# Optimization experiments

Measured on AMD Instinct MI355X. Metric: run time of the kernel, lower is better.

The kernel has to match this reference:

```python
import jax, jax.numpy as jnp
import numpy as np

_SCAN_CHUNK = 32


def _causal_decay_scan(x, decay, init):
    """Inclusive scan out[t] = decay*out[t-1] + x[t], chunked closed form.
    x: [B,H,T,D], decay: [1,H,1], init: [B,H,D]. Returns [B,H,T,D]."""
    B, H, T, D = x.shape
    C = min(_SCAN_CHUNK, T)
    assert T % C == 0
    nC = T // C
    log_decay = jnp.log(jnp.clip(decay.astype(jnp.float32), 1e-8, None))  # [1,H,1]
    c_idx = jnp.arange(C, dtype=jnp.float32)
    log_p = log_decay[..., None] * c_idx.reshape(1, 1, C, 1)              # [1,H,C,1]
    p = jnp.exp(log_p)
    inv_p = jnp.exp(-log_p)
    init_p = jnp.exp(log_decay[..., None] * (c_idx + 1.0).reshape(1, 1, C, 1))
    # [nC, B, H, C, D] so lax.scan chains chunk states causally
    xc = x.reshape(B, H, nC, C, D).transpose(2, 0, 1, 3, 4).astype(jnp.float32)

    def step(state, chunk):  # state [B,H,D], chunk [B,H,C,D]
        cs = jnp.cumsum(chunk * inv_p, axis=2)
        out = cs * p + state[:, :, None, :] * init_p
        return out[:, :, -1, :], out

    _, outs = jax.lax.scan(step, init.astype(jnp.float32), xc)
    return outs.transpose(1, 2, 0, 3, 4).reshape(B, H, T, D).astype(x.dtype)


def _phi(x):
    return jax.nn.elu(x) + 1.0


def setup_inputs() -> dict:
    key = jax.random.key(0)
    ks = jax.random.split(key, 5)
    B, T, hidden, H = 4, 4096, 1024, 16
    s = 1.0 / np.sqrt(hidden)
    x = jax.random.normal(ks[0], (B, T, hidden), dtype=jnp.float32)
    Wqkv = jax.random.normal(ks[1], (3 * hidden, hidden), dtype=jnp.float32) * s
    Wout = jax.random.normal(ks[2], (hidden, hidden), dtype=jnp.float32) * s
    Wgate = jax.random.normal(ks[3], (hidden, hidden), dtype=jnp.float32) * s
    bgate = jnp.zeros((hidden,), dtype=jnp.float32)
    logit = float(np.log(0.95 / 0.05))  # sigmoid(logit) == 0.95
    decay_param = jnp.full((H,), logit, dtype=jnp.float32)
    return {"x": x, "Wqkv": Wqkv, "Wout": Wout, "Wgate": Wgate,
            "bgate": bgate, "decay_param": decay_param}


def reference(x, Wqkv, Wout, Wgate, bgate, decay_param):
    B, T, hidden = x.shape
    H = decay_param.shape[0]
    D = hidden // H
    qkv = x @ Wqkv.T                       # [B,T,3*hidden]
    q, k, v = jnp.split(qkv, 3, axis=-1)
    # [B,T,hidden] -> [B,H,T,D]
    q = q.reshape(B, T, H, D).transpose(0, 2, 1, 3)
    k = k.reshape(B, T, H, D).transpose(0, 2, 1, 3)
    v = v.reshape(B, T, H, D).transpose(0, 2, 1, 3)
    q = _phi(q)
    k = _phi(k)
    decay = jax.nn.sigmoid(decay_param).reshape(1, H, 1)
    kv_init = jnp.zeros((B, H, D), dtype=x.dtype)
    ksum_init = jnp.zeros((B, H, D), dtype=x.dtype)
    running_kv = _causal_decay_scan(k * v, decay, kv_init)
    running_ksum = _causal_decay_scan(k, decay, ksum_init)
    den = jnp.clip(jnp.sum(q * running_ksum, axis=-1, keepdims=True), 1e-6, None)
    out = q * running_kv / den             # [B,H,T,D]
    v_direct = v.transpose(0, 2, 1, 3).reshape(B, T, hidden)
    out = out.transpose(0, 2, 1, 3).reshape(B, T, hidden)
    g = jax.nn.sigmoid(out @ Wgate.T + bgate)
    out = g * out + (1.0 - g) * v_direct
    return out @ Wout.T
```

## Files before the change

kernel.cpp:

```cpp
#include <hip/hip_runtime.h>

typedef unsigned short u16;
typedef __bf16 bf16x8 __attribute__((ext_vector_type(8)));
typedef float f32x4 __attribute__((ext_vector_type(4)));
typedef unsigned short us8 __attribute__((ext_vector_type(8)));

#define BB 4
#define TT 4096
#define HID 1024
#define NH 16
#define HD 64
#define BT (BB*TT)
#define NCH 128
#define LOG_NCH 7
#define CLEN (TT/NCH)

__device__ __forceinline__ float bf2f(u16 u) {
    return __uint_as_float(((unsigned)u) << 16);
}
__device__ __forceinline__ u16 f2bf(float f) {
    unsigned u = __float_as_uint(f);
    unsigned r = 0x7FFFu + ((u >> 16) & 1u);
    return (u16)((u + r) >> 16);
}
__device__ __forceinline__ float phi(float x) {
    return x > 0.f ? x + 1.f : __expf(x);
}
__device__ __forceinline__ float sigmoidf(float x) {
    return 1.f / (1.f + __expf(-x));
}
__device__ __forceinline__ float4 u4_to_f4(ushort4 u) {
    return make_float4(bf2f(u.x), bf2f(u.y), bf2f(u.z), bf2f(u.w));
}

#define CN1 (BT*HID/4)
#define CN2 (3*HID*HID/4)
#define CN3 (HID*HID/4)
#define CN4 (HID*HID/4)
__global__ void convert_all(const float4* __restrict__ x,    const float4* __restrict__ wqkv,
                            const float4* __restrict__ wgate, const float4* __restrict__ wout,
                            ushort4* __restrict__ xb,    ushort4* __restrict__ wqkvb,
                            ushort4* __restrict__ wgateb, ushort4* __restrict__ woutb) {
    int i = blockIdx.x * 256 + threadIdx.x;
    const float4* src; ushort4* dst; int j;
    if (i < CN1)                 { src = x;     dst = xb;     j = i; }
    else if (i < CN1+CN2)        { src = wqkv;  dst = wqkvb;  j = i - CN1; }
    else if (i < CN1+CN2+CN3)    { src = wgate; dst = wgateb; j = i - CN1 - CN2; }
    else                         { src = wout;  dst = woutb;  j = i - CN1 - CN2 - CN3; }
    float4 f = src[j];
    ushort4 u;
    u.x = f2bf(f.x); u.y = f2bf(f.y); u.z = f2bf(f.z); u.w = f2bf(f.w);
    dst[j] = u;
}

__global__ __launch_bounds__(256)
void gemm_bt(const u16* __restrict__ A, const u16* __restrict__ Bm,
             int M, int N, int K, u16* __restrict__ Cout)
{
    __shared__ u16 As[128 * 64];
    __shared__ u16 Bs[128 * 64];
    const int tid  = threadIdx.x;
    const int wave = tid >> 6;
    const int lane = tid & 63;

    const int lin   = blockIdx.y * gridDim.x + blockIdx.x;
    const int xcd   = lin & 7;
    const int seq   = lin >> 3;
    const int bands = gridDim.y >> 3;
    const int my_by = xcd * bands + (seq % bands);
    const int my_bx = seq / bands;
    const int m0 = my_by * 128;
    const int n0 = my_bx * 128;

    const int mw = (wave & 1) * 64;
    const int nw = (wave >> 1) * 64;
    const int r16 = lane & 15;
    const int q4  = (lane >> 4) * 4;

    f32x4 acc[4][4];
    #pragma unroll
    for (int i = 0; i < 4; ++i)
        #pragma unroll
        for (int j = 0; j < 4; ++j)
            acc[i][j] = (f32x4){0.f, 0.f, 0.f, 0.f};

    for (int k0 = 0; k0 < K; k0 += 64) {
        #pragma unroll
        for (int i = 0; i < 4; ++i) {
            int s   = i * 4 + wave;
            int idx = s * 64 + lane;
            int pr  = idx >> 3;
            int pc  = idx & 7;
            int lc  = pc ^ (pr & 7);
            const u16* gA = A  + (size_t)(m0 + pr) * K + k0 + lc * 8;
            const u16* gB = Bm + (size_t)(n0 + pr) * K + k0 + lc * 8;
            __builtin_amdgcn_global_load_lds(
                (const __attribute__((address_space(1))) void*)gA,
                (__attribute__((address_space(3))) void*)&As[s * 512], 16, 0, 0);
            __builtin_amdgcn_global_load_lds(
                (const __attribute__((address_space(1))) void*)gB,
                (__attribute__((address_space(3))) void*)&Bs[s * 512], 16, 0, 0);
        }
        __syncthreads();
        #pragma unroll
        for (int s2 = 0; s2 < 2; ++s2) {
            const int lcq = s2 * 4 + (lane >> 4);
            const int pcq = lcq ^ (r16 & 7);
            bf16x8 af[4], bq[4];
            #pragma unroll
            for (int i = 0; i < 4; ++i)
                af[i] = *(const bf16x8*)&As[(mw + i * 16 + r16) * 64 + pcq * 8];
            #pragma unroll
            for (int j = 0; j < 4; ++j)
                bq[j] = *(const bf16x8*)&Bs[(nw + j * 16 + r16) * 64 + pcq * 8];
            #pragma unroll
            for (int i = 0; i < 4; ++i)
                #pragma unroll
                for (int j = 0; j < 4; ++j)
                    acc[i][j] = __builtin_amdgcn_mfma_f32_16x16x32_bf16(af[i], bq[j], acc[i][j], 0, 0, 0);
        }
        __syncthreads();
    }

    float* Cs = (float*)As;
    #pragma unroll
    for (int slab = 0; slab < 4; ++slab) {
        if ((mw == 64) == (slab >= 2)) {
            int i0 = (slab & 1) * 2;
            #pragma unroll
            for (int ii = 0; ii < 2; ++ii) {
                #pragma unroll
                for (int j = 0; j < 4; ++j) {
                    int col = nw + j * 16 + r16;
                    #pragma unroll
                    for (int r = 0; r < 4; ++r)
                        Cs[(ii * 16 + q4 + r) * 128 + col] = acc[i0 + ii][j][r];
                }
            }
        }
        __syncthreads();
        #pragma unroll
        for (int s = 0; s < 2; ++s) {
            int g   = s * 256 + tid;
            int row = g >> 4;
            int cg  = g & 15;
            const float* cp = &Cs[row * 128 + cg * 8];
            us8 o;
            #pragma unroll
            for (int e = 0; e < 8; ++e) o[e] = f2bf(cp[e]);
            size_t grow = (size_t)(m0 + slab * 32 + row);
            *(us8*)&Cout[grow * N + n0 + cg * 8] = o;
        }
        __syncthreads();
    }
}

template<int EPI>
__global__ __launch_bounds__(256)
void gemm_bt_sm(const u16* __restrict__ A, const u16* __restrict__ Bm,
                int M, int N, int K, void* __restrict__ Cout,
                const float* __restrict__ bg,
                const u16* __restrict__ attn,
                const u16* __restrict__ qkv)
{
    __shared__ u16 As[64 * 64];
    __shared__ u16 Bs[128 * 64];
    const int tid  = threadIdx.x;
    const int wave = tid >> 6;
    const int lane = tid & 63;

    const int lin   = blockIdx.y * gridDim.x + blockIdx.x;
    const int xcd   = lin & 7;
    const int seq   = lin >> 3;
    const int bands = gridDim.y >> 3;
    const int my_by = xcd * bands + (seq % bands);
    const int my_bx = seq / bands;
    const int m0 = my_by * 64;
    const int n0 = my_bx * 128;

    const int mw = (wave & 1) * 32;
    const int nw = (wave >> 1) * 64;
    const int r16 = lane & 15;
    const int q4  = (lane >> 4) * 4;

    f32x4 acc[2][4];
    #pragma unroll
    for (int i = 0; i < 2; ++i)
        #pragma unroll
        for (int j = 0; j < 4; ++j)
            acc[i][j] = (f32x4){0.f, 0.f, 0.f, 0.f};

    for (int k0 = 0; k0 < K; k0 += 64) {
        #pragma unroll
        for (int i = 0; i < 4; ++i) {
            int s   = i * 4 + wave;
            int idx = s * 64 + lane;
            int pr  = idx >> 3;
            int pc  = idx & 7;
            int lc  = pc ^ (pr & 7);
            const u16* gB = Bm + (size_t)(n0 + pr) * K + k0 + lc * 8;
            __builtin_amdgcn_global_load_lds(
                (const __attribute__((address_space(1))) void*)gB,
                (__attribute__((address_space(3))) void*)&Bs[s * 512], 16, 0, 0);
            if (i < 2) {
                const u16* gA = A + (size_t)(m0 + pr) * K + k0 + lc * 8;
                __builtin_amdgcn_global_load_lds(
                    (const __attribute__((address_space(1))) void*)gA,
                    (__attribute__((address_space(3))) void*)&As[s * 512], 16, 0, 0);
            }
        }
        __syncthreads();
        #pragma unroll
        for (int s2 = 0; s2 < 2; ++s2) {
            const int lcq = s2 * 4 + (lane >> 4);
            const int pcq = lcq ^ (r16 & 7);
            bf16x8 af[2], bq[4];
            #pragma unroll
            for (int i = 0; i < 2; ++i)
                af[i] = *(const bf16x8*)&As[(mw + i * 16 + r16) * 64 + pcq * 8];
            #pragma unroll
            for (int j = 0; j < 4; ++j)
                bq[j] = *(const bf16x8*)&Bs[(nw + j * 16 + r16) * 64 + pcq * 8];
            #pragma unroll
            for (int i = 0; i < 2; ++i)
                #pragma unroll
                for (int j = 0; j < 4; ++j)
                    acc[i][j] = __builtin_amdgcn_mfma_f32_16x16x32_bf16(af[i], bq[j], acc[i][j], 0, 0, 0);
        }
        __syncthreads();
    }

    float* Cs = (float*)Bs;
    #pragma unroll
    for (int slab = 0; slab < 2; ++slab) {
        if ((wave & 1) == slab) {
            #pragma unroll
            for (int i = 0; i < 2; ++i) {
                #pragma unroll
                for (int j = 0; j < 4; ++j) {
                    int col = nw + j * 16 + r16;
                    #pragma unroll
                    for (int r = 0; r < 4; ++r)
                        Cs[(i * 16 + q4 + r) * 128 + col] = acc[i][j][r];
                }
            }
        }
        __syncthreads();
        #pragma unroll
        for (int s = 0; s < 2; ++s) {
            int g   = s * 256 + tid;
            int row = g >> 4;
            int cg  = g & 15;
            const float* cp = &Cs[row * 128 + cg * 8];
            size_t grow = (size_t)(m0 + slab * 32 + row);
            int gcol = n0 + cg * 8;
            if (EPI == 1) {
                us8 a8 = *(const us8*)&attn[grow * HID + gcol];
                us8 v8 = *(const us8*)&qkv[grow * (3 * HID) + 2 * HID + gcol];
                us8 o;
                #pragma unroll
                for (int e = 0; e < 8; ++e) {
                    float gv = sigmoidf(cp[e] + bg[gcol + e]);
                    o[e] = f2bf(gv * bf2f(a8[e]) + (1.f - gv) * bf2f(v8[e]));
                }
                *(us8*)&((u16*)Cout)[grow * HID + gcol] = o;
            } else {
                float4 c0 = *(const float4*)cp;
                float4 c1 = *(const float4*)(cp + 4);
                float* op = &((float*)Cout)[grow * N + gcol];
                *(float4*)op = c0;
                *(float4*)(op + 4) = c1;
            }
        }
        __syncthreads();
    }
}

__global__ void scan_finals(const u16* __restrict__ qkv, const float* __restrict__ decay_param,
                            float* __restrict__ ckv, float* __restrict__ cks) {
    int g  = blockIdx.x * 16 + (threadIdx.x >> 4);
    int sl = threadIdx.x & 15;
    int c = g & (NCH - 1);
    int h = (g >> LOG_NCH) & (NH - 1);
    int b = g >> (LOG_NCH + 4);
    float decay = sigmoidf(decay_param[h]);
    const u16* kp = qkv + (size_t)(b * TT + c * CLEN) * (3 * HID) + HID + h * HD + sl * 4;
    float4 skv = make_float4(0.f, 0.f, 0.f, 0.f);
    float4 sks = make_float4(0.f, 0.f, 0.f, 0.f);
    for (int t = 0; t < CLEN; ++t) {
        float4 k = u4_to_f4(*(const ushort4*)kp);
        float4 v = u4_to_f4(*(const ushort4*)(kp + HID));
        k.x = phi(k.x); k.y = phi(k.y); k.z = phi(k.z); k.w = phi(k.w);
        skv.x = decay * skv.x + k.x * v.x;  skv.y = decay * skv.y + k.y * v.y;
        skv.z = decay * skv.z + k.z * v.z;  skv.w = decay * skv.w + k.w * v.w;
        sks.x = decay * sks.x + k.x;        sks.y = decay * sks.y + k.y;
        sks.z = decay * sks.z + k.z;        sks.w = decay * sks.w + k.w;
        kp += 3 * HID;
    }
    *(float4*)(ckv + (size_t)g * 64 + sl * 4) = skv;
    *(float4*)(cks + (size_t)g * 64 + sl * 4) = sks;
}

__global__ void scan_prefix(float* __restrict__ ckv, float* __restrict__ cks,
                            const float* __restrict__ decay_param) {
    int bh = blockIdx.x;
    int h  = bh & (NH - 1);
    int lane = threadIdx.x;
    float decay = sigmoidf(decay_param[h]);
    float dC = powf(decay, (float)CLEN);
    float* pkv = ckv + (size_t)bh * NCH * 64 + lane;
    float* pks = cks + (size_t)bh * NCH * 64 + lane;
    float fkv = 0.f, fks = 0.f;
    for (int c = 0; c < NCH; ++c) {
        float lkv = pkv[c * 64], lks = pks[c * 64];
        pkv[c * 64] = fkv; pks[c * 64] = fks;
        fkv = fkv * dC + lkv;
        fks = fks * dC + lks;
    }
}

__global__ void scan_apply(const u16* __restrict__ qkv, const float* __restrict__ decay_param,
                           const float* __restrict__ ckv, const float* __restrict__ cks,
                           u16* __restrict__ attn) {
    int g  = blockIdx.x * 16 + (threadIdx.x >> 4);
    int sl = threadIdx.x & 15;
    int c = g & (NCH - 1);
    int h = (g >> LOG_NCH) & (NH - 1);
    int b = g >> (LOG_NCH + 4);
    float decay = sigmoidf(decay_param[h]);
    float4 skv = *(const float4*)(ckv + (size_t)g * 64 + sl * 4);
    float4 sks = *(const float4*)(cks + (size_t)g * 64 + sl * 4);
    const u16* qp = qkv + (size_t)(b * TT + c * CLEN) * (3 * HID) + h * HD + sl * 4;
    u16* op = attn + (size_t)(b * TT + c * CLEN) * HID + h * HD + sl * 4;
    for (int t = 0; t < CLEN; ++t) {
        float4 q = u4_to_f4(*(const ushort4*)qp);
        float4 k = u4_to_f4(*(const ushort4*)(qp + HID));
        float4 v = u4_to_f4(*(const ushort4*)(qp + 2 * HID));
        q.x = phi(q.x); q.y = phi(q.y); q.z = phi(q.z); q.w = phi(q.w);
        k.x = phi(k.x); k.y = phi(k.y); k.z = phi(k.z); k.w = phi(k.w);
        skv.x = decay * skv.x + k.x * v.x;  skv.y = decay * skv.y + k.y * v.y;
        skv.z = decay * skv.z + k.z * v.z;  skv.w = decay * skv.w + k.w * v.w;
        sks.x = decay * sks.x + k.x;        sks.y = decay * sks.y + k.y;
        sks.z = decay * sks.z + k.z;        sks.w = decay * sks.w + k.w;
        float s = q.x * sks.x + q.y * sks.y + q.z * sks.z + q.w * sks.w;
        s += __shfl_xor(s, 8);
        s += __shfl_xor(s, 4);
        s += __shfl_xor(s, 2);
        s += __shfl_xor(s, 1);
        float inv = 1.f / fmaxf(s, 1e-6f);
        ushort4 o;
        o.x = f2bf(q.x * skv.x * inv); o.y = f2bf(q.y * skv.y * inv);
        o.z = f2bf(q.z * skv.z * inv); o.w = f2bf(q.w * skv.w * inv);
        *(ushort4*)op = o;
        qp += 3 * HID;
        op += HID;
    }
}

extern "C" void kernel_launch(void* const* d_in, const int* in_sizes, int n_in,
                              void* d_out, int out_size, void* d_ws, size_t ws_size,
                              hipStream_t stream) {
    const float* x     = (const float*)d_in[0];
    const float* Wqkv  = (const float*)d_in[1];
    const float* Wout  = (const float*)d_in[2];
    const float* Wgate = (const float*)d_in[3];
    const float* bgate = (const float*)d_in[4];
    const float* decay = (const float*)d_in[5];

    u16* xb     = (u16*)d_ws;
    u16* wqkvb  = xb    + (size_t)BT * HID;
    u16* wgateb = wqkvb + (size_t)3 * HID * HID;
    u16* woutb  = wgateb + (size_t)HID * HID;
    u16* qkvb   = woutb + (size_t)HID * HID;
    u16* out2b  = qkvb  + (size_t)BT * 3 * HID;
    float* ckv  = (float*)(out2b + (size_t)BT * HID);
    float* cks  = ckv + (size_t)BB * NH * NCH * HD;
    u16* attnb  = xb;

    convert_all<<<(CN1 + CN2 + CN3 + CN4) / 256, 256, 0, stream>>>(
        (const float4*)x, (const float4*)Wqkv, (const float4*)Wgate, (const float4*)Wout,
        (ushort4*)xb, (ushort4*)wqkvb, (ushort4*)wgateb, (ushort4*)woutb);

    gemm_bt<<<dim3(3 * HID / 128, BT / 128), 256, 0, stream>>>(
        xb, wqkvb, BT, 3 * HID, HID, qkvb);

    scan_finals<<<BB * NH * NCH / 16, 256, 0, stream>>>(qkvb, decay, ckv, cks);
    scan_prefix<<<BB * NH, 64, 0, stream>>>(ckv, cks, decay);
    scan_apply<<<BB * NH * NCH / 16, 256, 0, stream>>>(qkvb, decay, ckv, cks, attnb);

    gemm_bt_sm<1><<<dim3(HID / 128, BT / 64), 256, 0, stream>>>(
        attnb, wgateb, BT, HID, HID, out2b, bgate, attnb, qkvb);

    gemm_bt_sm<2><<<dim3(HID / 128, BT / 64), 256, 0, stream>>>(
        out2b, woutb, BT, HID, HID, d_out, nullptr, nullptr, nullptr);
}
```

Measured before the change: 423.5 us.

## Drop XCD block remap, write GEMM output directly, widen K tile to 128

Both GEMM kernels drop the XCD-aware block-index remapping and use plain blockIdx tile coordinates. The QKV GEMM replaces its LDS-staged, vectorized bf16 epilogue with direct per-element stores from the accumulators, which removes shared-memory round trips and barriers but leaves the global writes narrow. The small-M GEMM doubles its K tile to 128, halving loop iterations and barriers at the cost of more LDS. It also pads the C staging stride to cut bank conflicts and loads the gate bias as float4 vectors. Losing the remap may reduce L2 locality across XCDs.

```diff
diff --git a/kernel.cpp b/kernel.cpp
--- a/kernel.cpp
+++ b/kernel.cpp
@@ -62,20 +62,11 @@
     const int tid  = threadIdx.x;
     const int wave = tid >> 6;
     const int lane = tid & 63;
-
-    const int lin   = blockIdx.y * gridDim.x + blockIdx.x;
-    const int xcd   = lin & 7;
-    const int seq   = lin >> 3;
-    const int bands = gridDim.y >> 3;
-    const int my_by = xcd * bands + (seq % bands);
-    const int my_bx = seq / bands;
-    const int m0 = my_by * 128;
-    const int n0 = my_bx * 128;
-
+    const int m0 = blockIdx.y * 128;
+    const int n0 = blockIdx.x * 128;
     const int mw = (wave & 1) * 64;
     const int nw = (wave >> 1) * 64;
     const int r16 = lane & 15;
-    const int q4  = (lane >> 4) * 4;
 
     f32x4 acc[4][4];
     #pragma unroll
@@ -122,39 +113,20 @@
         __syncthreads();
     }
 
-    float* Cs = (float*)As;
     #pragma unroll
-    for (int slab = 0; slab < 4; ++slab) {
-        if ((mw == 64) == (slab >= 2)) {
-            int i0 = (slab & 1) * 2;
-            #pragma unroll
-            for (int ii = 0; ii < 2; ++ii) {
-                #pragma unroll
-                for (int j = 0; j < 4; ++j) {
-                    int col = nw + j * 16 + r16;
-                    #pragma unroll
-                    for (int r = 0; r < 4; ++r)
-                        Cs[(ii * 16 + q4 + r) * 128 + col] = acc[i0 + ii][j][r];
-                }
-            }
-        }
-        __syncthreads();
-        #pragma unroll
-        for (int s = 0; s < 2; ++s) {
-            int g   = s * 256 + tid;
-            int row = g >> 4;
-            int cg  = g & 15;
-            const float* cp = &Cs[row * 128 + cg * 8];
-            us8 o;
-            #pragma unroll
-            for (int e = 0; e < 8; ++e) o[e] = f2bf(cp[e]);
-            size_t grow = (size_t)(m0 + slab * 32 + row);
-            *(us8*)&Cout[grow * N + n0 + cg * 8] = o;
-        }
-        __syncthreads();
-    }
-}
-
+    for (int i = 0; i < 4; ++i) {
+        int rowb = m0 + mw + i * 16 + (lane >> 4) * 4;
+        #pragma unroll
+        for (int j = 0; j < 4; ++j) {
+            int col = n0 + nw + j * 16 + r16;
+            #pragma unroll
+            for (int r = 0; r < 4; ++r)
+                Cout[(size_t)(rowb + r) * N + col] = f2bf(acc[i][j][r]);
+        }
+    }
+}
+
+#define CS_LD 132
 template<int EPI>
 __global__ __launch_bounds__(256)
 void gemm_bt_sm(const u16* __restrict__ A, const u16* __restrict__ Bm,
@@ -163,21 +135,13 @@
                 const u16* __restrict__ attn,
                 const u16* __restrict__ qkv)
 {
-    __shared__ u16 As[64 * 64];
-    __shared__ u16 Bs[128 * 64];
+    __shared__ u16 As[64 * 128];
+    __shared__ u16 Bs[128 * 128];
     const int tid  = threadIdx.x;
     const int wave = tid >> 6;
     const int lane = tid & 63;
-
-    const int lin   = blockIdx.y * gridDim.x + blockIdx.x;
-    const int xcd   = lin & 7;
-    const int seq   = lin >> 3;
-    const int bands = gridDim.y >> 3;
-    const int my_by = xcd * bands + (seq % bands);
-    const int my_bx = seq / bands;
-    const int m0 = my_by * 64;
-    const int n0 = my_bx * 128;
-
+    const int m0 = blockIdx.y * 64;
+    const int n0 = blockIdx.x * 128;
     const int mw = (wave & 1) * 32;
     const int nw = (wave >> 1) * 64;
     const int r16 = lane & 15;
@@ -190,19 +154,19 @@
         for (int j = 0; j < 4; ++j)
             acc[i][j] = (f32x4){0.f, 0.f, 0.f, 0.f};
 
-    for (int k0 = 0; k0 < K; k0 += 64) {
-        #pragma unroll
-        for (int i = 0; i < 4; ++i) {
+    for (int k0 = 0; k0 < K; k0 += 128) {
+        #pragma unroll
+        for (int i = 0; i < 8; ++i) {
             int s   = i * 4 + wave;
             int idx = s * 64 + lane;
-            int pr  = idx >> 3;
-            int pc  = idx & 7;
+            int pr  = idx >> 4;
+            int pc  = idx & 15;
             int lc  = pc ^ (pr & 7);
             const u16* gB = Bm + (size_t)(n0 + pr) * K + k0 + lc * 8;
             __builtin_amdgcn_global_load_lds(
                 (const __attribute__((address_space(1))) void*)gB,
                 (__attribute__((address_space(3))) void*)&Bs[s * 512], 16, 0, 0);
-            if (i < 2) {
+            if (i < 4) {
                 const u16* gA = A + (size_t)(m0 + pr) * K + k0 + lc * 8;
                 __builtin_amdgcn_global_load_lds(
                     (const __attribute__((address_space(1))) void*)gA,
@@ -211,16 +175,16 @@
         }
         __syncthreads();
         #pragma unroll
-        for (int s2 = 0; s2 < 2; ++s2) {
+        for (int s2 = 0; s2 < 4; ++s2) {
             const int lcq = s2 * 4 + (lane >> 4);
             const int pcq = lcq ^ (r16 & 7);
             bf16x8 af[2], bq[4];
             #pragma unroll
             for (int i = 0; i < 2; ++i)
-                af[i] = *(const bf16x8*)&As[(mw + i * 16 + r16) * 64 + pcq * 8];
+                af[i] = *(const bf16x8*)&As[(mw + i * 16 + r16) * 128 + pcq * 8];
             #pragma unroll
             for (int j = 0; j < 4; ++j)
-                bq[j] = *(const bf16x8*)&Bs[(nw + j * 16 + r16) * 64 + pcq * 8];
+                bq[j] = *(const bf16x8*)&Bs[(nw + j * 16 + r16) * 128 + pcq * 8];
             #pragma unroll
             for (int i = 0; i < 2; ++i)
                 #pragma unroll
@@ -241,7 +205,7 @@
                     int col = nw + j * 16 + r16;
                     #pragma unroll
                     for (int r = 0; r < 4; ++r)
-                        Cs[(i * 16 + q4 + r) * 128 + col] = acc[i][j][r];
+                        Cs[(i * 16 + q4 + r) * CS_LD + col] = acc[i][j][r];
                 }
             }
         }
@@ -251,16 +215,19 @@
             int g   = s * 256 + tid;
             int row = g >> 4;
             int cg  = g & 15;
-            const float* cp = &Cs[row * 128 + cg * 8];
+            const float* cp = &Cs[row * CS_LD + cg * 8];
             size_t grow = (size_t)(m0 + slab * 32 + row);
             int gcol = n0 + cg * 8;
             if (EPI == 1) {
                 us8 a8 = *(const us8*)&attn[grow * HID + gcol];
                 us8 v8 = *(const us8*)&qkv[grow * (3 * HID) + 2 * HID + gcol];
+                float4 b0 = *(const float4*)&bg[gcol];
+                float4 b1 = *(const float4*)&bg[gcol + 4];
+                float bb[8] = {b0.x, b0.y, b0.z, b0.w, b1.x, b1.y, b1.z, b1.w};
                 us8 o;
                 #pragma unroll
                 for (int e = 0; e < 8; ++e) {
-                    float gv = sigmoidf(cp[e] + bg[gcol + e]);
+                    float gv = sigmoidf(cp[e] + bb[e]);
                     o[e] = f2bf(gv * bf2f(a8[e]) + (1.f - gv) * bf2f(v8[e]));
                 }
                 *(us8*)&((u16*)Cout)[grow * HID + gcol] = o;
```

Result: faster. 405.9 us (-4.1%).
